# Performance work log

Measured on AMD Instinct MI355X. Metric: run time of the kernel, lower is better.

Reference implementation:

```python
import jax, jax.numpy as jnp
import numpy as np

B, H, A, D = 4096, 50, 32, 64          # batch, history len, neighbor count, embed_dim
NU, NV = 100000, 100000                # num users, num items
L = H + A                              # total gathered entries per node


def setup_inputs() -> dict:
    key = jax.random.key(0)
    ks = jax.random.split(key, 16)
    # embedding tables (u2e/v2e uniform(-1,1) as in module init, r2e ~ N(0,1) default)
    u2e = jax.random.uniform(ks[0], (NU, D), minval=-1.0, maxval=1.0, dtype=jnp.float32)
    v2e = jax.random.uniform(ks[1], (NV, D), minval=-1.0, maxval=1.0, dtype=jnp.float32)
    r2e = jax.random.normal(ks[2], (7, D), dtype=jnp.float32)
    relation_att = jax.random.normal(ks[3], (2 * D,), dtype=jnp.float32)
    s = 1.0 / np.sqrt(2 * D)  # torch Linear default init bound
    agg_W = jax.random.uniform(ks[4], (D, 2 * D), minval=-s, maxval=s, dtype=jnp.float32)
    agg_b = jax.random.uniform(ks[5], (D,), minval=-s, maxval=s, dtype=jnp.float32)
    lin1_W = jax.random.uniform(ks[6], (D, 2 * D), minval=-s, maxval=s, dtype=jnp.float32)
    lin1_b = jax.random.uniform(ks[7], (D,), minval=-s, maxval=s, dtype=jnp.float32)
    nodes_u = jax.random.randint(ks[8], (B,), 0, NU)
    nodes_v = jax.random.randint(ks[9], (B,), 0, NV)
    hist_u = jax.random.randint(ks[10], (B, H), 0, NV)   # user history = items
    hist_ur = jax.random.randint(ks[11], (B, H), 0, 6)   # ratings 0..5
    adj_u = jax.random.randint(ks[12], (B, A), 0, NU)    # social neighbors = users
    hist_v = jax.random.randint(ks[13], (B, H), 0, NU)   # item history = users
    hist_vr = jax.random.randint(ks[14], (B, H), 0, 6)
    adj_v = jax.random.randint(ks[15], (B, A), 0, NV)    # item-adj neighbors = items
    return dict(u2e=u2e, v2e=v2e, r2e=r2e, relation_att=relation_att,
                agg_W=agg_W, agg_b=agg_b, lin1_W=lin1_W, lin1_b=lin1_b,
                nodes_u=nodes_u, nodes_v=nodes_v,
                hist_u=hist_u, hist_ur=hist_ur, adj_u=adj_u,
                hist_v=hist_v, hist_vr=hist_vr, adj_v=adj_v)


def _encode(node_tab, target_tab, hist_tab, neigh_tab, r2e, relation_att,
            agg_W, agg_b, lin1_W, lin1_b, nodes, targets, hn, hr, adj):
    # Node_Encoder.forward + Node_Aggregator (percent=1.0 -> deterministic:
    # multinomial selects all indices; softmax-weighted sum is permutation-invariant).
    nf = node_tab[nodes]                                   # [B, D]
    tf = target_tab[targets]                               # [B, D]
    # query (computed as in original; with percent=1 the norm-softmax sampling
    # probability does not affect the output)
    _q = jnp.concatenate([nf, tf], axis=-1) @ agg_W.T + agg_b  # [B, D]
    hist_feat = jnp.concatenate([hist_tab[hn], neigh_tab[adj]], axis=1)  # [B, L, D]
    rates = jnp.concatenate([hr, jnp.full(adj.shape, 6, dtype=hr.dtype)], axis=1)
    rate_feat = r2e[rates]                                 # [B, L, D]
    sel = jnp.concatenate([hist_feat, rate_feat], axis=-1)  # [B, L, 2D]
    logits = jnp.einsum('ble,e->bl', sel, relation_att)    # [B, L]
    p = jax.nn.softmax(logits, axis=1)                     # softmax2 over entries
    neigh = jnp.einsum('bl,bld->bd', p, hist_feat)         # weighted sum [B, D]
    comb = jnp.concatenate([nf, neigh], axis=-1)           # [B, 2D]
    return jax.nn.relu(comb @ lin1_W.T + lin1_b)           # [B, D]


def reference(u2e, v2e, r2e, relation_att, agg_W, agg_b, lin1_W, lin1_b,
              nodes_u, nodes_v, hist_u, hist_ur, adj_u, hist_v, hist_vr, adj_v):
    # user side: isitem=False -> node=u2e, target=v2e, hist=v2e, neighbor=u2e
    eu = _encode(u2e, v2e, v2e, u2e, r2e, relation_att, agg_W, agg_b, lin1_W, lin1_b,
                 nodes_u, nodes_v, hist_u, hist_ur, adj_u)
    # item side: isitem=True -> node=v2e, target=u2e, hist=u2e, neighbor=v2e
    ev = _encode(v2e, u2e, u2e, v2e, r2e, relation_att, agg_W, agg_b, lin1_W, lin1_b,
                 nodes_v, nodes_u, hist_v, hist_vr, adj_v)
    return jnp.sum(eu * ev, axis=1)                        # [B]
```

## Files before the change

kernel.cpp:

```cpp
#include <hip/hip_runtime.h>


#define NB 4096
#define NH 50
#define NA 32
#define ND 64

__global__ void rlog_setup(const float* __restrict__ r2e,
                           const float* __restrict__ ra,
                           float* __restrict__ ws_rlog)
{
    const int lane = threadIdx.x;
    const float ra_hi = ra[64 + lane];
    #pragma unroll
    for (int r = 0; r < 7; ++r) {
        float part = r2e[r * 64 + lane] * ra_hi;
        #pragma unroll
        for (int off = 32; off >= 1; off >>= 1)
            part += __shfl_xor(part, off);
        if (lane == 0) ws_rlog[r] = part;
    }
}

__global__ __launch_bounds__(256, 8) void graphconsis_main(
    const float* __restrict__ u2e, const float* __restrict__ v2e,
    const float* __restrict__ ra,
    const float* __restrict__ lin1_W, const float* __restrict__ lin1_b,
    const int* __restrict__ nodes_u, const int* __restrict__ nodes_v,
    const int* __restrict__ hist_u, const int* __restrict__ hist_ur,
    const int* __restrict__ adj_u,
    const int* __restrict__ hist_v, const int* __restrict__ hist_vr,
    const int* __restrict__ adj_v,
    const float* __restrict__ ws_rlog,
    float* __restrict__ out)
{
    __shared__ float lds_comb[4][128];
    __shared__ float ed[4][64];

    const int wid  = threadIdx.x >> 6;
    const int lane = threadIdx.x & 63;
    const int side = wid >> 1;
    const int b    = __builtin_amdgcn_readfirstlane(blockIdx.x * 2 + (wid & 1));

    const float* nodeTab  = side ? v2e : u2e;
    const float* histTab  = side ? u2e : v2e;
    const float* neighTab = side ? v2e : u2e;
    const int* nodes = side ? nodes_v : nodes_u;
    const int* hn    = side ? hist_v  : hist_u;
    const int* hr    = side ? hist_vr : hist_ur;
    const int* adj   = side ? adj_v   : adj_u;

    const float ra_lo = ra[lane];
    const float rlog6 = ws_rlog[6];

    const float nf = nodeTab[nodes[b] * ND + lane];

    float rl0 = 0.f;
    if (lane < NH) rl0 = ws_rlog[hr[b * NH + lane]];

    float ssum = 0.f, acc = 0.f;

    #pragma unroll 10
    for (int l = 0; l < NH; ++l) {
        const int idx = hn[b * NH + l];
        const float e = histTab[idx * ND + lane];
        float part = fmaf(e, ra_lo, (lane == l) ? rl0 : 0.f);
        #pragma unroll
        for (int off = 32; off >= 1; off >>= 1)
            part += __shfl_xor(part, off);
        const float p = __expf(part);
        ssum += p;
        acc = fmaf(p, e, acc);
    }
    #pragma unroll 8
    for (int l = 0; l < NA; ++l) {
        const int idx = adj[b * NA + l];
        const float e = neighTab[idx * ND + lane];
        float part = e * ra_lo;
        #pragma unroll
        for (int off = 32; off >= 1; off >>= 1)
            part += __shfl_xor(part, off);
        const float p = __expf(part + rlog6);
        ssum += p;
        acc = fmaf(p, e, acc);
    }
    const float neigh = acc / ssum;

    lds_comb[wid][lane]      = nf;
    lds_comb[wid][64 + lane] = neigh;

    float o = lin1_b[lane];
    const float4* W4 = (const float4*)(lin1_W + lane * 128);
    const float4* C4 = (const float4*)lds_comb[wid];
    #pragma unroll 8
    for (int kk = 0; kk < 32; ++kk) {
        const float4 w = W4[kk];
        const float4 c = C4[kk];
        o = fmaf(w.x, c.x, o);
        o = fmaf(w.y, c.y, o);
        o = fmaf(w.z, c.z, o);
        o = fmaf(w.w, c.w, o);
    }
    const float evec = fmaxf(o, 0.f);

    ed[wid][lane] = evec;
    __syncthreads();

    if (wid < 2) {
        float prod = ed[wid][lane] * ed[wid + 2][lane];
        #pragma unroll
        for (int off = 32; off >= 1; off >>= 1)
            prod += __shfl_xor(prod, off);
        if (lane == 0) out[blockIdx.x * 2 + wid] = prod;
    }
}

extern "C" void kernel_launch(void* const* d_in, const int* in_sizes, int n_in,
                              void* d_out, int out_size, void* d_ws, size_t ws_size,
                              hipStream_t stream)
{
    const float* u2e     = (const float*)d_in[0];
    const float* v2e     = (const float*)d_in[1];
    const float* r2e     = (const float*)d_in[2];
    const float* ra      = (const float*)d_in[3];
    const float* lin1_W  = (const float*)d_in[6];
    const float* lin1_b  = (const float*)d_in[7];
    const int* nodes_u   = (const int*)d_in[8];
    const int* nodes_v   = (const int*)d_in[9];
    const int* hist_u    = (const int*)d_in[10];
    const int* hist_ur   = (const int*)d_in[11];
    const int* adj_u     = (const int*)d_in[12];
    const int* hist_v    = (const int*)d_in[13];
    const int* hist_vr   = (const int*)d_in[14];
    const int* adj_v     = (const int*)d_in[15];
    float* out = (float*)d_out;
    float* ws_rlog = (float*)d_ws;

    hipLaunchKernelGGL(rlog_setup, dim3(1), dim3(64), 0, stream, r2e, ra, ws_rlog);
    hipLaunchKernelGGL(graphconsis_main, dim3(NB / 2), dim3(256), 0, stream,
                       u2e, v2e, ra, lin1_W, lin1_b,
                       nodes_u, nodes_v, hist_u, hist_ur, adj_u,
                       hist_v, hist_vr, adj_v, ws_rlog, out);
}
```

Measured before the change: 63.48 us.

## Process four gathered embeddings per wavefront using 16-lane groups with float4 loads

Each wavefront is split into four 16-lane groups, and each group handles a different history or neighbor entry per iteration, loading rows as float4. The history indices are preloaded into registers. The per-entry dot-product reduction now takes four shuffles instead of six. The partial softmax sums and weighted accumulators are combined across groups at the end. The aim is to cut shuffle and loop overhead and raise memory-level parallelism on the random-row gathers, at the cost of more registers and an extra cross-group reduction.

```diff
diff --git a/kernel.cpp b/kernel.cpp
--- a/kernel.cpp
+++ b/kernel.cpp
@@ -39,6 +39,8 @@
 
     const int wid  = threadIdx.x >> 6;
     const int lane = threadIdx.x & 63;
+    const int g    = lane >> 4;
+    const int j    = lane & 15;
     const int side = wid >> 1;
     const int b    = __builtin_amdgcn_readfirstlane(blockIdx.x * 2 + (wid & 1));
 
@@ -50,44 +52,93 @@
     const int* hr    = side ? hist_vr : hist_ur;
     const int* adj   = side ? adj_v   : adj_u;
 
-    const float ra_lo = ra[lane];
+    const float4 ra4  = *(const float4*)(ra + 4 * j);
     const float rlog6 = ws_rlog[6];
 
-    const float nf = nodeTab[nodes[b] * ND + lane];
+    int hidx[13];
+    #pragma unroll
+    for (int k = 0; k < 13; ++k) {
+        int l = 4 * k + g; if (l > NH - 1) l = NH - 1;
+        hidx[k] = hn[b * NH + l];
+    }
+    float rl0 = 0.f;
+    { int l = 4 * j + g; if (l < NH) rl0 = ws_rlog[hr[b * NH + l]]; }
 
-    float rl0 = 0.f;
-    if (lane < NH) rl0 = ws_rlog[hr[b * NH + lane]];
+    float ssum = 0.f;
+    float4 acc = make_float4(0.f, 0.f, 0.f, 0.f);
 
-    float ssum = 0.f, acc = 0.f;
-
-    #pragma unroll 10
-    for (int l = 0; l < NH; ++l) {
-        const int idx = hn[b * NH + l];
-        const float e = histTab[idx * ND + lane];
-        float part = fmaf(e, ra_lo, (lane == l) ? rl0 : 0.f);
-        #pragma unroll
-        for (int off = 32; off >= 1; off >>= 1)
-            part += __shfl_xor(part, off);
+    #pragma unroll 4
+    for (int k = 0; k < 12; ++k) {
+        const float4 e = *(const float4*)(histTab + hidx[k] * ND + 4 * j);
+        float part = e.x * ra4.x;
+        part = fmaf(e.y, ra4.y, part);
+        part = fmaf(e.z, ra4.z, part);
+        part = fmaf(e.w, ra4.w, part);
+        part += (j == k) ? rl0 : 0.f;
+        part += __shfl_xor(part, 1);
+        part += __shfl_xor(part, 2);
+        part += __shfl_xor(part, 4);
+        part += __shfl_xor(part, 8);
         const float p = __expf(part);
         ssum += p;
-        acc = fmaf(p, e, acc);
+        acc.x = fmaf(p, e.x, acc.x);
+        acc.y = fmaf(p, e.y, acc.y);
+        acc.z = fmaf(p, e.z, acc.z);
+        acc.w = fmaf(p, e.w, acc.w);
     }
-    #pragma unroll 8
-    for (int l = 0; l < NA; ++l) {
-        const int idx = adj[b * NA + l];
-        const float e = neighTab[idx * ND + lane];
-        float part = e * ra_lo;
-        #pragma unroll
-        for (int off = 32; off >= 1; off >>= 1)
-            part += __shfl_xor(part, off);
+    {
+        const float4 e = *(const float4*)(histTab + hidx[12] * ND + 4 * j);
+        float part = e.x * ra4.x;
+        part = fmaf(e.y, ra4.y, part);
+        part = fmaf(e.z, ra4.z, part);
+        part = fmaf(e.w, ra4.w, part);
+        part += (j == 12) ? rl0 : 0.f;
+        part += __shfl_xor(part, 1);
+        part += __shfl_xor(part, 2);
+        part += __shfl_xor(part, 4);
+        part += __shfl_xor(part, 8);
+        const float p = (g < 2) ? __expf(part) : 0.f;
+        ssum += p;
+        acc.x = fmaf(p, e.x, acc.x);
+        acc.y = fmaf(p, e.y, acc.y);
+        acc.z = fmaf(p, e.z, acc.z);
+        acc.w = fmaf(p, e.w, acc.w);
+    }
+    #pragma unroll 4
+    for (int k = 0; k < 8; ++k) {
+        const int idx = adj[b * NA + 4 * k + g];
+        const float4 e = *(const float4*)(neighTab + idx * ND + 4 * j);
+        float part = e.x * ra4.x;
+        part = fmaf(e.y, ra4.y, part);
+        part = fmaf(e.z, ra4.z, part);
+        part = fmaf(e.w, ra4.w, part);
+        part += __shfl_xor(part, 1);
+        part += __shfl_xor(part, 2);
+        part += __shfl_xor(part, 4);
+        part += __shfl_xor(part, 8);
         const float p = __expf(part + rlog6);
         ssum += p;
-        acc = fmaf(p, e, acc);
+        acc.x = fmaf(p, e.x, acc.x);
+        acc.y = fmaf(p, e.y, acc.y);
+        acc.z = fmaf(p, e.z, acc.z);
+        acc.w = fmaf(p, e.w, acc.w);
     }
-    const float neigh = acc / ssum;
 
-    lds_comb[wid][lane]      = nf;
-    lds_comb[wid][64 + lane] = neigh;
+    ssum += __shfl_xor(ssum, 16);
+    ssum += __shfl_xor(ssum, 32);
+    acc.x += __shfl_xor(acc.x, 16); acc.x += __shfl_xor(acc.x, 32);
+    acc.y += __shfl_xor(acc.y, 16); acc.y += __shfl_xor(acc.y, 32);
+    acc.z += __shfl_xor(acc.z, 16); acc.z += __shfl_xor(acc.z, 32);
+    acc.w += __shfl_xor(acc.w, 16); acc.w += __shfl_xor(acc.w, 32);
+
+    const float inv = 1.0f / ssum;
+    const float4 nf4 = *(const float4*)(nodeTab + nodes[b] * ND + 4 * j);
+
+    if (g == 0) {
+        *(float4*)&lds_comb[wid][4 * j] = nf4;
+        float4 n4 = make_float4(acc.x * inv, acc.y * inv, acc.z * inv, acc.w * inv);
+        *(float4*)&lds_comb[wid][64 + 4 * j] = n4;
+    }
 
     float o = lin1_b[lane];
     const float4* W4 = (const float4*)(lin1_W + lane * 128);
```

Measured after the change: 59.13 us. -6.8%, faster.
